# Optimization experiments

Measured on AMD Instinct MI355X. Metric: run time of the kernel, lower is better.

The kernel has to match this reference:

```python
import jax, jax.numpy as jnp
import numpy as np

# ---- config constants (must match init_kwargs) ----
B, S, D, H, HD = 2, 2048, 512, 8, 64
N_BLK, L_BLK = 64, 32          # block_size, block_len (S = N_BLK*L_BLK)
R, RM = 8, 4                   # router_size, group_router_mul_factor
LN, GN, GE, GT = 8, 4, 16, 2   # moe layers, groups, group experts, topk per token
DR, DG = 128, 128
FFH = 1024
THETA = 10000.0
EPS = 1e-6

_INV_FREQ = (1.0 / THETA) ** (np.arange(0, HD, 2, dtype=np.float32) / HD)


def rmsnorm(x, w):
    return x * jax.lax.rsqrt(jnp.mean(x * x, axis=-1, keepdims=True) + EPS) * w


def rope(x):
    # x: (b, h, s, hd); y1 = x1*cos + x2*sin, y2 = -x1*sin + x2*cos (as in RotaryEmb)
    s = x.shape[2]
    freqs = jnp.outer(jnp.arange(s, dtype=jnp.float32), jnp.asarray(_INV_FREQ))[None, None]
    cos, sin = jnp.cos(freqs), jnp.sin(freqs)
    x1, x2 = jnp.split(x, 2, axis=-1)
    return jnp.concatenate([x1 * cos + x2 * sin, -x1 * sin + x2 * cos], axis=-1)


def layer(x, mask, qkv_w, o_w, up_w, down_w, n1, n2):
    b, s, d = x.shape
    xn = rmsnorm(x, n1)
    q, k, v = jnp.split(xn @ qkv_w, 3, axis=-1)
    sh = lambda t: t.reshape(b, s, H, HD).transpose(0, 2, 1, 3)  # b h s hd
    q, k, v = rope(sh(q)), rope(sh(k)), sh(v)
    scores = jnp.einsum('bhqa,bhka->bhqk', q, k) / np.sqrt(HD).astype(np.float32)
    if mask is not None:
        scores = jnp.where(mask[:, None], scores, -jnp.inf)
    p = jax.nn.softmax(scores, axis=-1)
    o = jnp.einsum('bhqk,bhka->bhqa', p, v).transpose(0, 2, 1, 3).reshape(b, s, d)
    x = x + o @ o_w
    xn2 = rmsnorm(x, n2)
    h1, h2 = jnp.split(xn2 @ up_w, 2, axis=-1)
    return x + (jax.nn.silu(h1) * h2) @ down_w


def _l2n(t, axis):
    return t / jnp.maximum(jnp.linalg.norm(t, axis=axis, keepdims=True), 1e-12)


def forward(x, doc, router_token, out_w, keys_router, keys_gate,
            enc_qkv, enc_o, enc_up, enc_down, enc_n1, enc_n2,
            rtr_qkv, rtr_o, rtr_up, rtr_down, rtr_n1, rtr_n2):
    # ---- AuxEncoder: block-causal AND same-document mask (global_attn branch) ----
    qb = jnp.arange(S) // N_BLK
    causal = qb[:, None] >= qb[None, :]                       # (S, S)
    mask = causal[None] & (doc[:, :, None] == doc[:, None, :])  # (B, S, S)
    for i in range(enc_qkv.shape[0]):
        x = layer(x, mask, enc_qkv[i], enc_o[i], enc_up[i], enc_down[i], enc_n1[i], enc_n2[i])

    # ---- AuxRouter: split into blocks, append router tokens, full attention ----
    xr = x.reshape(B * L_BLK, N_BLK, D)
    rt = jnp.broadcast_to(router_token, (B * L_BLK, R, D))
    xr = jnp.concatenate([xr, rt], axis=1)                    # (B*L, N+R, D)
    for i in range(rtr_qkv.shape[0]):
        xr = layer(xr, None, rtr_qkv[i], rtr_o[i], rtr_up[i], rtr_down[i], rtr_n1[i], rtr_n2[i])
    out = xr[:, N_BLK:] @ out_w                               # (B*L, R, DR+DG)
    xro, xgo = out[..., :DR], out[..., DR:]

    def expand(t, dd):
        # repeat '(b l) r d -> (r rm) b l d', roll(1, dim=2), flatten(1,2)
        t = t.reshape(B, L_BLK, R, dd).transpose(2, 0, 1, 3)  # (R, B, L, d)
        t = jnp.repeat(t, RM, axis=0)                          # (R*RM, B, L, d)
        t = jnp.roll(t, 1, axis=2)
        return t.reshape(R * RM, B * L_BLK, dd)

    xrr = _l2n(expand(xro, DR), -1)
    xgg = _l2n(expand(xgo, DG), -1)
    kr = _l2n(keys_router, 1)
    kg = _l2n(keys_gate, 1)
    rl = jnp.einsum('gbd,gde->gbe', xrr, kr)                  # (LN*GN, B*L, GE)
    gl = jnp.einsum('gbd,gde->gbe', xgg, kg)
    _, idx = jax.lax.top_k(rl, GT)                            # (LN*GN, B*L, GT)
    rv = jnp.take_along_axis(rl, idx, axis=-1)
    gv = jnp.take_along_axis(gl, idx, axis=-1)
    return jnp.stack([rv, gv], axis=0)                        # (2, 32, 64, 2)


def setup_inputs() -> dict:
    key = jax.random.key(0)
    ks = jax.random.split(key, 20)
    w = lambda k, shp: 0.02 * jax.random.normal(k, shp, dtype=jnp.float32)
    return {
        'x': jax.random.normal(ks[0], (B, S, D), dtype=jnp.float32),
        'doc': jnp.sort(jax.random.randint(ks[1], (B, S), 0, 4), axis=-1),
        'router_token': jax.random.normal(ks[2], (1, R, D), dtype=jnp.float32),
        'out_w': w(ks[3], (D, DR + DG)),
        'keys_router': jax.random.normal(ks[4], (LN * GN, DR, GE), dtype=jnp.float32),
        'keys_gate': jax.random.normal(ks[5], (LN * GN, DG, GE), dtype=jnp.float32),
        'enc_qkv': w(ks[6], (4, D, 3 * D)),
        'enc_o': w(ks[7], (4, D, D)),
        'enc_up': w(ks[8], (4, D, 2 * FFH)),
        'enc_down': w(ks[9], (4, FFH, D)),
        'enc_n1': jnp.ones((4, D), dtype=jnp.float32),
        'enc_n2': jnp.ones((4, D), dtype=jnp.float32),
        'rtr_qkv': w(ks[10], (2, D, 3 * D)),
        'rtr_o': w(ks[11], (2, D, D)),
        'rtr_up': w(ks[12], (2, D, 2 * FFH)),
        'rtr_down': w(ks[13], (2, FFH, D)),
        'rtr_n1': jnp.ones((2, D), dtype=jnp.float32),
        'rtr_n2': jnp.ones((2, D), dtype=jnp.float32),
    }


def reference(x, doc, router_token, out_w, keys_router, keys_gate,
              enc_qkv, enc_o, enc_up, enc_down, enc_n1, enc_n2,
              rtr_qkv, rtr_o, rtr_up, rtr_down, rtr_n1, rtr_n2):
    return forward(x, doc, router_token, out_w, keys_router, keys_gate,
                   enc_qkv, enc_o, enc_up, enc_down, enc_n1, enc_n2,
                   rtr_qkv, rtr_o, rtr_up, rtr_down, rtr_n1, rtr_n2)
```

## Files before the change

### kernel.cpp

```cpp
#include <hip/hip_runtime.h>
#include <hip/hip_bf16.h>
#include <cstdint>


typedef __attribute__((ext_vector_type(8))) short short8;
typedef __attribute__((ext_vector_type(4))) float f32x4;
typedef unsigned short ushort_t;

__device__ __forceinline__ float bf2f(unsigned short u) {
    return __uint_as_float(((unsigned)u) << 16);
}
__device__ __forceinline__ unsigned short f2bf(float f) {
    unsigned u = __float_as_uint(f);
    unsigned r = 0x7FFFu + ((u >> 16) & 1u);
    return (unsigned short)((u + r) >> 16);
}
__device__ __forceinline__ float wave_sum64(float v) {
#pragma unroll
    for (int o = 32; o; o >>= 1) v += __shfl_xor(v, o);
    return v;
}
__device__ __forceinline__ void load_lds16(const ushort_t* g, ushort_t* l) {
    __builtin_amdgcn_global_load_lds(
        (const __attribute__((address_space(1))) unsigned int*)g,
        (__attribute__((address_space(3))) unsigned int*)l, 16, 0, 0);
}

#define MFMA16(a, b, c) __builtin_amdgcn_mfma_f32_16x16x32_bf16(a, b, c, 0, 0, 0)
#define BARRIER_RAW() do { asm volatile("" ::: "memory"); \
    __builtin_amdgcn_s_barrier(); asm volatile("" ::: "memory"); } while (0)
#define VMCNT0() asm volatile("s_waitcnt vmcnt(0)" ::: "memory")

__global__ void copy_in_kernel(const float* __restrict__ src,
                               float* __restrict__ dst, int n) {
    int i = blockIdx.x * 256 + threadIdx.x;
    if (i < n) dst[i] = src[i];
}

__global__ __launch_bounds__(256) void wsplit_kernel(const float* __restrict__ W,
        unsigned short* __restrict__ WH, unsigned short* __restrict__ WL,
        int K, int N) {
    __shared__ float tile[32][33];
    int bn = blockIdx.x * 32, bk = blockIdx.y * 32;
    int tx = threadIdx.x & 31, ty = threadIdx.x >> 5;
#pragma unroll
    for (int i = 0; i < 4; ++i)
        tile[ty + 8 * i][tx] = W[(size_t)(bk + ty + 8 * i) * N + bn + tx];
    __syncthreads();
#pragma unroll
    for (int i = 0; i < 4; ++i) {
        int n = bn + ty + 8 * i, k = bk + tx;
        float x = tile[tx][ty + 8 * i];
        unsigned short h = f2bf(x);
        unsigned short lo = f2bf(x - bf2f(h));
        WH[(size_t)n * K + k] = h;
        WL[(size_t)n * K + k] = lo;
    }
}

__global__ __launch_bounds__(256) void rmsnorm_kernel(const float* __restrict__ X,
        const float* __restrict__ W, ushort_t* __restrict__ XNH,
        ushort_t* __restrict__ XNL) {
    int t = blockIdx.x, tid = threadIdx.x;
    const float* xr = X + (size_t)t * 512;
    float v0 = xr[tid], v1 = xr[tid + 256];
    float ss = wave_sum64(v0 * v0 + v1 * v1);
    __shared__ float red[4];
    if ((tid & 63) == 0) red[tid >> 6] = ss;
    __syncthreads();
    float tot = red[0] + red[1] + red[2] + red[3];
    float scale = rsqrtf(tot * (1.0f / 512.0f) + 1e-6f);
    float a0 = v0 * scale * W[tid];
    float a1 = v1 * scale * W[tid + 256];
    unsigned short h0 = f2bf(a0), h1 = f2bf(a1);
    size_t base = (size_t)t * 512;
    XNH[base + tid]       = h0;
    XNL[base + tid]       = f2bf(a0 - bf2f(h0));
    XNH[base + tid + 256] = h1;
    XNL[base + tid + 256] = f2bf(a1 - bf2f(h1));
}

template <int BM>
__global__ __launch_bounds__(256) void gemm3(
        const ushort_t* __restrict__ AH, const ushort_t* __restrict__ AL,
        const ushort_t* __restrict__ BH, const ushort_t* __restrict__ BL,
        const float* __restrict__ Res, float* __restrict__ C,
        int M, int N, int K) {
    constexpr int MI   = BM / 32;
    constexpr int ROWS = 2 * BM + 256;
    constexpr int LPW  = ROWS / 64;
    constexpr int SS   = ROWS * 32;
    __shared__ __align__(16) ushort_t S[2][ROWS][32];
    int tid = threadIdx.x;
    int n0 = blockIdx.x * 128, m0 = blockIdx.y * BM;
    int wid = tid >> 6, lane = tid & 63;
    int wm = (wid >> 1) * (BM / 2), wn = (wid & 1) * 64;
    int col = lane & 15, quad = lane >> 4;

    const ushort_t* gsrc[LPW];
    int ldof[LPW];
#pragma unroll
    for (int j = 0; j < LPW; ++j) {
        int e = wid * LPW + j;
        int srow = e * 16 + (lane >> 2);
        const ushort_t* gp; int rin;
        if (srow < BM)                { gp = AH + (size_t)m0 * K; rin = srow; }
        else if (srow < 2 * BM)       { gp = AL + (size_t)m0 * K; rin = srow - BM; }
        else if (srow < 2 * BM + 128) { gp = BH + (size_t)n0 * K; rin = srow - 2 * BM; }
        else                          { gp = BL + (size_t)n0 * K; rin = srow - 2 * BM - 128; }
        gsrc[j] = gp + (size_t)rin * K + ((lane & 3) ^ ((lane >> 3) & 3)) * 8;
        ldof[j] = e * 512;
    }
    ushort_t* sbase = &S[0][0][0];
    auto STAGE = [&](int set, int kc) {
        ushort_t* sb = sbase + set * SS;
#pragma unroll
        for (int j = 0; j < LPW; ++j)
            load_lds16(gsrc[j] + kc * 32, sb + ldof[j]);
    };

    int chrd = (quad ^ ((col >> 1) & 3)) * 8;
    f32x4 acc[MI][4] = {};
    int nk = K >> 5;
    STAGE(0, 0);
    VMCNT0();
    BARRIER_RAW();
    int cur = 0;
#pragma unroll 1
    for (int kc = 0; kc < nk; ++kc) {
        if (kc + 1 < nk) STAGE(cur ^ 1, kc + 1);
        const ushort_t* sb = sbase + cur * SS;
        short8 afh[MI], afl[MI], bfh[4], bfl[4];
#pragma unroll
        for (int i = 0; i < MI; ++i) {
            afh[i] = *(const short8*)(sb + (size_t)(wm + i * 16 + col) * 32 + chrd);
            afl[i] = *(const short8*)(sb + (size_t)(BM + wm + i * 16 + col) * 32 + chrd);
        }
#pragma unroll
        for (int i = 0; i < 4; ++i) {
            bfh[i] = *(const short8*)(sb + (size_t)(2 * BM + wn + i * 16 + col) * 32 + chrd);
            bfl[i] = *(const short8*)(sb + (size_t)(2 * BM + 128 + wn + i * 16 + col) * 32 + chrd);
        }
#pragma unroll
        for (int mi = 0; mi < MI; ++mi)
#pragma unroll
            for (int ni = 0; ni < 4; ++ni) {
                f32x4 c = acc[mi][ni];
                c = MFMA16(afh[mi], bfh[ni], c);
                c = MFMA16(afh[mi], bfl[ni], c);
                c = MFMA16(afl[mi], bfh[ni], c);
                acc[mi][ni] = c;
            }
        if (kc + 1 < nk) {
            VMCNT0();
            BARRIER_RAW();
            cur ^= 1;
        }
    }
#pragma unroll
    for (int mi = 0; mi < MI; ++mi)
#pragma unroll
        for (int ni = 0; ni < 4; ++ni)
#pragma unroll
            for (int r = 0; r < 4; ++r) {
                int row = m0 + wm + mi * 16 + quad * 4 + r;
                int ccol = n0 + wn + ni * 16 + col;
                size_t o = (size_t)row * N + ccol;
                float v = acc[mi][ni][r];
                if (Res) v += Res[o];
                C[o] = v;
            }
}

__global__ __launch_bounds__(256) void gemm_up_silu(
        const ushort_t* __restrict__ AH, const ushort_t* __restrict__ AL,
        const ushort_t* __restrict__ BH, const ushort_t* __restrict__ BL,
        ushort_t* __restrict__ MIDH, ushort_t* __restrict__ MIDL, int K) {
    constexpr int ROWS = 640;
    constexpr int LPW  = 10;
    constexpr int SS   = ROWS * 32;
    __shared__ __align__(16) ushort_t S[2][ROWS][32];
    int tid = threadIdx.x;
    int n0 = blockIdx.x * 128, m0 = blockIdx.y * 64;
    int wid = tid >> 6, lane = tid & 63;
    int wm = (wid >> 1) * 32, wn = (wid & 1) * 64;
    int col = lane & 15, quad = lane >> 4;

    const ushort_t* gsrc[LPW];
    int ldof[LPW];
#pragma unroll
    for (int j = 0; j < LPW; ++j) {
        int e = wid * LPW + j;
        int srow = e * 16 + (lane >> 2);
        const ushort_t* gp; int rin;
        if (srow < 64)       { gp = AH; rin = m0 + srow; }
        else if (srow < 128) { gp = AL; rin = m0 + srow - 64; }
        else if (srow < 256) { gp = BH; rin = n0 + srow - 128; }
        else if (srow < 384) { gp = BL; rin = n0 + srow - 256; }
        else if (srow < 512) { gp = BH; rin = 1024 + n0 + srow - 384; }
        else                 { gp = BL; rin = 1024 + n0 + srow - 512; }
        gsrc[j] = gp + (size_t)rin * K + ((lane & 3) ^ ((lane >> 3) & 3)) * 8;
        ldof[j] = e * 512;
    }
    ushort_t* sbase = &S[0][0][0];
    auto STAGE = [&](int set, int kc) {
        ushort_t* sb = sbase + set * SS;
#pragma unroll
        for (int j = 0; j < LPW; ++j)
            load_lds16(gsrc[j] + kc * 32, sb + ldof[j]);
    };

    int chrd = (quad ^ ((col >> 1) & 3)) * 8;
    f32x4 a1[2][4] = {}, a2[2][4] = {};
    int nk = K >> 5;
    STAGE(0, 0);
    VMCNT0();
    BARRIER_RAW();
    int cur = 0;
#pragma unroll 1
    for (int kc = 0; kc < nk; ++kc) {
        if (kc + 1 < nk) STAGE(cur ^ 1, kc + 1);
        const ushort_t* sb = sbase + cur * SS;
        short8 afh[2], afl[2], b1h[4], b1l[4], b2h[4], b2l[4];
#pragma unroll
        for (int i = 0; i < 2; ++i) {
            afh[i] = *(const short8*)(sb + (size_t)(wm + i * 16 + col) * 32 + chrd);
            afl[i] = *(const short8*)(sb + (size_t)(64 + wm + i * 16 + col) * 32 + chrd);
        }
#pragma unroll
        for (int i = 0; i < 4; ++i) {
            b1h[i] = *(const short8*)(sb + (size_t)(128 + wn + i * 16 + col) * 32 + chrd);
            b1l[i] = *(const short8*)(sb + (size_t)(256 + wn + i * 16 + col) * 32 + chrd);
            b2h[i] = *(const short8*)(sb + (size_t)(384 + wn + i * 16 + col) * 32 + chrd);
            b2l[i] = *(const short8*)(sb + (size_t)(512 + wn + i * 16 + col) * 32 + chrd);
        }
#pragma unroll
        for (int mi = 0; mi < 2; ++mi)
#pragma unroll
            for (int ni = 0; ni < 4; ++ni) {
                f32x4 c = a1[mi][ni];
                c = MFMA16(afh[mi], b1h[ni], c);
                c = MFMA16(afh[mi], b1l[ni], c);
                c = MFMA16(afl[mi], b1h[ni], c);
                a1[mi][ni] = c;
                f32x4 d = a2[mi][ni];
                d = MFMA16(afh[mi], b2h[ni], d);
                d = MFMA16(afh[mi], b2l[ni], d);
                d = MFMA16(afl[mi], b2h[ni], d);
                a2[mi][ni] = d;
            }
        if (kc + 1 < nk) {
            VMCNT0();
            BARRIER_RAW();
            cur ^= 1;
        }
    }
#pragma unroll
    for (int mi = 0; mi < 2; ++mi)
#pragma unroll
        for (int ni = 0; ni < 4; ++ni)
#pragma unroll
            for (int r = 0; r < 4; ++r) {
                int row = m0 + wm + mi * 16 + quad * 4 + r;
                int ccol = n0 + wn + ni * 16 + col;
                float v1 = a1[mi][ni][r], v2 = a2[mi][ni][r];
                float rr = (v1 / (1.0f + __expf(-v1))) * v2;
                unsigned short h = f2bf(rr);
                size_t o = (size_t)row * 1024 + ccol;
                MIDH[o] = h;
                MIDL[o] = f2bf(rr - bf2f(h));
            }
}

__global__ void rope_pack_kernel(const float* __restrict__ QKV,
        float* __restrict__ Q, ushort_t* __restrict__ KH,
        ushort_t* __restrict__ KL, int Sg, int total) {
    int idx = blockIdx.x * 256 + threadIdx.x;
    if (idx >= total) return;
    int i = idx & 31;
    int h = (idx >> 5) & 7;
    int t = idx >> 8;
    int g = t / Sg; int s = t - g * Sg;
    const float* row = QKV + (size_t)t * 1536;
    float inv = powf(10000.0f, -(float)(2 * i) / 64.0f);
    float sn, cs;
    sincosf((float)s * inv, &sn, &cs);
    size_t ob = ((size_t)(g * 8 + h) * Sg + s) * 64 + i;
    int c = h * 64 + i;
    float q1 = row[c], q2 = row[c + 32];
    Q[ob]      = q1 * cs + q2 * sn;
    Q[ob + 32] = q2 * cs - q1 * sn;
    float k1 = row[512 + c], k2 = row[512 + c + 32];
    float ka = k1 * cs + k2 * sn;
    float kb = k2 * cs - k1 * sn;
    unsigned short ha = f2bf(ka), hb = f2bf(kb);
    KH[ob]      = ha;  KL[ob]      = f2bf(ka - bf2f(ha));
    KH[ob + 32] = hb;  KL[ob + 32] = f2bf(kb - bf2f(hb));
}

__global__ __launch_bounds__(256) void vtrans_kernel(const float* __restrict__ QKV,
        ushort_t* __restrict__ VTH, ushort_t* __restrict__ VTL, int Sg) {
    __shared__ float tile[64][65];
    int chunk = blockIdx.x, gh = blockIdx.y;
    int g = gh >> 3, h = gh & 7;
    int tid = threadIdx.x;
    int sr = tid >> 2, dc = (tid & 3) * 16;
    int s = chunk * 64 + sr;
    if (s < Sg) {
        const float* src = QKV + ((size_t)g * Sg + s) * 1536 + 1024 + h * 64 + dc;
#pragma unroll
        for (int j = 0; j < 4; ++j) {
            float4 v = *(const float4*)(src + 4 * j);
            tile[sr][dc + 4 * j]     = v.x;
            tile[sr][dc + 4 * j + 1] = v.y;
            tile[sr][dc + 4 * j + 2] = v.z;
            tile[sr][dc + 4 * j + 3] = v.w;
        }
    } else {
#pragma unroll
        for (int j = 0; j < 16; ++j) tile[sr][dc + j] = 0.f;
    }
    __syncthreads();
    int dr = tid >> 2, sc = (tid & 3) * 16;
    short8 hv[2], lv[2];
#pragma unroll
    for (int half = 0; half < 2; ++half)
#pragma unroll
        for (int j = 0; j < 8; ++j) {
            float v = tile[sc + half * 8 + j][dr];
            unsigned short hb = f2bf(v);
            hv[half][j] = (short)hb;
            lv[half][j] = (short)f2bf(v - bf2f(hb));
        }
    int scol = chunk * 64 + sc;
    size_t ob = ((size_t)gh * 64 + dr) * Sg + scol;
    if (scol + 16 <= Sg) {
        *(short8*)(VTH + ob)     = hv[0];
        *(short8*)(VTH + ob + 8) = hv[1];
        *(short8*)(VTL + ob)     = lv[0];
        *(short8*)(VTL + ob + 8) = lv[1];
    } else {
#pragma unroll
        for (int j = 0; j < 16; ++j)
            if (scol + j < Sg) {
                VTH[ob + j] = (ushort_t)((j < 8) ? hv[0][j] : hv[1][j - 8]);
                VTL[ob + j] = (ushort_t)((j < 8) ? lv[0][j] : lv[1][j - 8]);
            }
    }
}

template <bool MASKED>
__global__ __launch_bounds__(256, 3) void attn3_kernel(const float* __restrict__ Q,
        const ushort_t* __restrict__ KHg, const ushort_t* __restrict__ KLg,
        const ushort_t* __restrict__ VTHg, const ushort_t* __restrict__ VTLg,
        const int* __restrict__ doc, ushort_t* __restrict__ AOH,
        ushort_t* __restrict__ AOL, int Sg) {
    __shared__ __align__(16) ushort_t Khs[64][64], Kls[64][64];
    __shared__ __align__(16) ushort_t Vts[64][64], Vtl[64][64];
    __shared__ __align__(16) ushort_t Ph[4][16][72], Pl[4][16][72];
    __shared__ int dock[64];
    int qb = (int)(gridDim.x - 1 - blockIdx.x);
    int gh = blockIdx.y, g = gh >> 3;
    int tid = threadIdx.x, wid = tid >> 6, lane = tid & 63;
    int col = lane & 15, quad = lane >> 4;

    int rL = lane >> 3, cSw = (lane & 7) ^ rL;
    const ushort_t* kb;
    const ushort_t* vb;
    ushort_t* lb;
    if (wid == 0)      { kb = KHg + (size_t)gh * Sg * 64 + cSw * 8;  vb = nullptr; lb = &Khs[0][0]; }
    else if (wid == 1) { kb = KLg + (size_t)gh * Sg * 64 + cSw * 8;  vb = nullptr; lb = &Kls[0][0]; }
    else if (wid == 2) { vb = VTHg + ((size_t)gh * 64 + rL) * Sg;    kb = nullptr; lb = &Vts[0][0]; }
    else               { vb = VTLg + ((size_t)gh * 64 + rL) * Sg;    kb = nullptr; lb = &Vtl[0][0]; }
    int sw0 = ((0 + quad) ^ (col & 7)) * 8;
    int sw1 = ((4 + quad) ^ (col & 7)) * 8;

    short8 qa[2][2];
    {
        int qrow = qb * 64 + wid * 16 + col;
        if (qrow >= Sg) qrow = Sg - 1;
        const float* Qg = Q + ((size_t)gh * Sg + qrow) * 64 + quad * 8;
#pragma unroll
        for (int kk = 0; kk < 2; ++kk) {
            float4 v0 = *(const float4*)(Qg + kk * 32);
            float4 v1 = *(const float4*)(Qg + kk * 32 + 4);
            float vv[8] = {v0.x, v0.y, v0.z, v0.w, v1.x, v1.y, v1.z, v1.w};
            short8 h, l;
#pragma unroll
            for (int e = 0; e < 8; ++e) {
                float x = vv[e] * 0.125f;
                unsigned short hb = f2bf(x);
                h[e] = (short)hb;
                l[e] = (short)f2bf(x - bf2f(hb));
            }
            qa[kk][0] = h; qa[kk][1] = l;
        }
    }
    int dqr[4]; int wq0 = 0, wq1 = 0, bq0 = 0, bq1 = 0;
    if (MASKED) {
        const int* db = doc + (size_t)g * Sg + qb * 64;
#pragma unroll
        for (int r = 0; r < 4; ++r) dqr[r] = db[wid * 16 + quad * 4 + r];
        wq0 = db[wid * 16]; wq1 = db[wid * 16 + 15];
        bq0 = db[0];        bq1 = db[63];
    }
    float m[4], l[4];
    f32x4 accO[4];
#pragma unroll
    for (int r = 0; r < 4; ++r) { m[r] = -1e30f; l[r] = 0.f; }
#pragma unroll
    for (int nd = 0; nd < 4; ++nd) accO[nd] = (f32x4){0.f, 0.f, 0.f, 0.f};

    int nkt = MASKED ? (qb + 1) : ((Sg + 63) >> 6);
    for (int kt = 0; kt < nkt; ++kt) {
        int kval = Sg - kt * 64; if (kval > 64) kval = 64;
        __syncthreads();
        if (MASKED) {
            if (tid < 64) dock[tid] = doc[(size_t)g * Sg + kt * 64 + tid];
            __syncthreads();
        }
        bool bskip = false;
        if (MASKED) bskip = (dock[63] < bq0) || (dock[0] > bq1);
        if (!bskip) {
            if (wid < 2) {
#pragma unroll
                for (int p = 0; p < 8; ++p) {
                    int sr2 = kt * 64 + p * 8 + rL;
                    if (sr2 > Sg - 1) sr2 = Sg - 1;
                    load_lds16(kb + (size_t)sr2 * 64, lb + p * 512);
                }
            } else {
                int vc = kt * 64 + cSw * 8;
                if (vc > Sg - 8) vc = Sg - 8;
#pragma unroll
                for (int p = 0; p < 8; ++p)
                    load_lds16(vb + (size_t)(p * 8) * Sg + vc, lb + p * 512);
            }
            __syncthreads();
            bool wskip = false;
            if (MASKED) wskip = (dock[kval - 1] < wq0) || (dock[0] > wq1);
            if (!wskip) {
                int dk[4];
                if (MASKED) {
#pragma unroll
                    for (int ni = 0; ni < 4; ++ni) dk[ni] = dock[ni * 16 + col];
                }
                f32x4 sc[4];
#pragma unroll
                for (int ni = 0; ni < 4; ++ni) {
                    int rb = (ni * 16 + col) * 64;
                    short8 bh0 = *(const short8*)(&Khs[0][0] + rb + sw0);
                    short8 bl0 = *(const short8*)(&Kls[0][0] + rb + sw0);
                    short8 bh1 = *(const short8*)(&Khs[0][0] + rb + sw1);
                    short8 bl1 = *(const short8*)(&Kls[0][0] + rb + sw1);
                    f32x4 c = (f32x4){0.f, 0.f, 0.f, 0.f};
                    c = MFMA16(qa[0][0], bh0, c);
                    c = MFMA16(qa[0][0], bl0, c);
                    c = MFMA16(qa[0][1], bh0, c);
                    c = MFMA16(qa[1][0], bh1, c);
                    c = MFMA16(qa[1][0], bl1, c);
                    c = MFMA16(qa[1][1], bh1, c);
                    sc[ni] = c;
                }
                float mnew[4];
#pragma unroll
                for (int r = 0; r < 4; ++r) mnew[r] = -1e30f;
#pragma unroll
                for (int ni = 0; ni < 4; ++ni)
#pragma unroll
                    for (int r = 0; r < 4; ++r) {
                        bool ok = MASKED ? (dk[ni] == dqr[r]) : (ni * 16 + col < kval);
                        float s = ok ? sc[ni][r] : -1e30f;
                        sc[ni][r] = s;
                        mnew[r] = fmaxf(mnew[r], s);
                    }
#pragma unroll
                for (int r = 0; r < 4; ++r)
#pragma unroll
                    for (int o = 1; o < 16; o <<= 1)
                        mnew[r] = fmaxf(mnew[r], __shfl_xor(mnew[r], o));
                float alpha[4], lsum[4];
#pragma unroll
                for (int r = 0; r < 4; ++r) {
                    float M = fmaxf(m[r], mnew[r]);
                    alpha[r] = __expf(m[r] - M);
                    m[r] = M;
                    lsum[r] = 0.f;
                }
#pragma unroll
                for (int ni = 0; ni < 4; ++ni)
#pragma unroll
                    for (int r = 0; r < 4; ++r) {
                        bool ok = MASKED ? (dk[ni] == dqr[r]) : (ni * 16 + col < kval);
                        float p = ok ? __expf(sc[ni][r] - m[r]) : 0.f;
                        lsum[r] += p;
                        unsigned short h = f2bf(p);
                        Ph[wid][quad * 4 + r][ni * 16 + col] = h;
                        Pl[wid][quad * 4 + r][ni * 16 + col] = f2bf(p - bf2f(h));
                    }
#pragma unroll
                for (int r = 0; r < 4; ++r) {
#pragma unroll
                    for (int o = 1; o < 16; o <<= 1)
                        lsum[r] += __shfl_xor(lsum[r], o);
                    l[r] = l[r] * alpha[r] + lsum[r];
                }
#pragma unroll
                for (int nd = 0; nd < 4; ++nd)
#pragma unroll
                    for (int r = 0; r < 4; ++r) accO[nd][r] *= alpha[r];
#pragma unroll
                for (int kk = 0; kk < 2; ++kk) {
                    short8 pah = *(const short8*)&Ph[wid][col][kk * 32 + quad * 8];
                    short8 pal = *(const short8*)&Pl[wid][col][kk * 32 + quad * 8];
                    int sw = kk ? sw1 : sw0;
#pragma unroll
                    for (int nd = 0; nd < 4; ++nd) {
                        int rb = (nd * 16 + col) * 64;
                        short8 vbh = *(const short8*)(&Vts[0][0] + rb + sw);
                        short8 vbl = *(const short8*)(&Vtl[0][0] + rb + sw);
                        f32x4 c = accO[nd];
                        c = MFMA16(pah, vbh, c);
                        c = MFMA16(pah, vbl, c);
                        c = MFMA16(pal, vbh, c);
                        accO[nd] = c;
                    }
                }
            }
        }
    }
#pragma unroll
    for (int r = 0; r < 4; ++r) {
        int qrow = qb * 64 + wid * 16 + quad * 4 + r;
        if (qrow < Sg) {
            float inv = 1.0f / l[r];
            size_t base = ((size_t)g * Sg + qrow) * 512 + (gh & 7) * 64;
#pragma unroll
            for (int nd = 0; nd < 4; ++nd) {
                float val = accO[nd][r] * inv;
                unsigned short h = f2bf(val);
                AOH[base + nd * 16 + col] = h;
                AOL[base + nd * 16 + col] = f2bf(val - bf2f(h));
            }
        }
    }
}

__global__ void router_build_kernel(const float* __restrict__ X,
        const float* __restrict__ RT, float* __restrict__ X2, int total) {
    int idx = blockIdx.x * 256 + threadIdx.x;
    if (idx >= total) return;
    int d = idx & 511;
    int p = (idx >> 9) % 72;
    int g2 = idx / (72 * 512);
    X2[idx] = (p < 64) ? X[((size_t)g2 * 64 + p) * 512 + d]
                       : RT[(p - 64) * 512 + d];
}

__global__ void gather_rows_kernel(const float* __restrict__ X2,
        ushort_t* __restrict__ RRH, ushort_t* __restrict__ RRL, int total) {
    int idx = blockIdx.x * 256 + threadIdx.x;
    if (idx >= total) return;
    int d = idx & 511;
    int row = idx >> 9;
    int g2 = row >> 3, rr = row & 7;
    float v = X2[((size_t)(g2 * 72 + 64 + rr)) * 512 + d];
    unsigned short h = f2bf(v);
    RRH[idx] = h;
    RRL[idx] = f2bf(v - bf2f(h));
}

__global__ __launch_bounds__(64) void norm_half_kernel(const float* __restrict__ IN,
        float* __restrict__ OUT) {
    int b = blockIdx.x; int lane = threadIdx.x;
    size_t base = (size_t)(b >> 1) * 256 + (size_t)(b & 1) * 128;
    float v0 = IN[base + lane], v1 = IN[base + 64 + lane];
    float ss = wave_sum64(v0 * v0 + v1 * v1);
    float sc = 1.0f / fmaxf(sqrtf(ss), 1e-12f);
    OUT[base + lane]      = v0 * sc;
    OUT[base + 64 + lane] = v1 * sc;
}

__global__ __launch_bounds__(64) void norm_keys_kernel(const float* __restrict__ Kin,
        float* __restrict__ Kout) {
    int b = blockIdx.x; int lane = threadIdx.x;
    int g = b >> 4, e = b & 15;
    size_t base = (size_t)g * 2048 + e;
    float v0 = Kin[base + (size_t)lane * 16];
    float v1 = Kin[base + (size_t)(lane + 64) * 16];
    float ss = wave_sum64(v0 * v0 + v1 * v1);
    float sc = 1.0f / fmaxf(sqrtf(ss), 1e-12f);
    Kout[base + (size_t)lane * 16]        = v0 * sc;
    Kout[base + (size_t)(lane + 64) * 16] = v1 * sc;
}

__global__ __launch_bounds__(64) void logits_top2_kernel(const float* __restrict__ OUTN,
        const float* __restrict__ KRN, const float* __restrict__ KGN,
        float* __restrict__ out) {
    int blk = blockIdx.x;
    int g = blk >> 6, bcol = blk & 63;
    int b = bcol >> 5, l = bcol & 31;
    int lsrc = (l + 31) & 31;
    int r = g >> 2;
    int row = (b * 32 + lsrc) * 8 + r;
    const float* rvec = OUTN + (size_t)row * 256;
    __shared__ float sc[32];
    int lane = threadIdx.x;
    if (lane < 32) {
        int e = lane & 15;
        const float* kb = ((lane < 16) ? KRN : KGN) + (size_t)g * 2048 + e;
        const float* xv = (lane < 16) ? rvec : (rvec + 128);
        float s = 0.f;
#pragma unroll 8
        for (int d = 0; d < 128; ++d) s = fmaf(xv[d], kb[(size_t)d * 16], s);
        sc[lane] = s;
    }
    __syncthreads();
    if (lane == 0) {
        float bv = -1e30f, sv = -1e30f; int bi = 0, si = 0;
#pragma unroll
        for (int e = 0; e < 16; ++e) {
            float v = sc[e];
            if (v > bv) { sv = bv; si = bi; bv = v; bi = e; }
            else if (v > sv) { sv = v; si = e; }
        }
        size_t base = (size_t)g * 128 + (size_t)bcol * 2;
        out[base]            = bv;
        out[base + 1]        = sv;
        out[4096 + base]     = sc[16 + bi];
        out[4096 + base + 1] = sc[16 + si];
    }
}

static void run_layer(float* X, float* BIG, float* Qb,
                      ushort_t* KHb, ushort_t* KLb, ushort_t* VTHb, ushort_t* VTLb,
                      ushort_t* XNH, ushort_t* XNL, ushort_t* AOH, ushort_t* AOL,
                      ushort_t* MIDH, ushort_t* MIDL,
                      const unsigned short* WH, const unsigned short* WL,
                      const float* n1, const float* n2,
                      const int* doc, int G, int Sg, hipStream_t stream) {
    const size_t oQKV = 0, oO = 786432, oUP = 1048576, oDN = 2097152;
    int T = G * Sg;
    rmsnorm_kernel<<<T, 256, 0, stream>>>(X, n1, XNH, XNL);
    gemm3<64><<<dim3(12, T / 64), 256, 0, stream>>>(XNH, XNL, WH + oQKV, WL + oQKV, nullptr, BIG, T, 1536, 512);
    int rp = T * 256;
    rope_pack_kernel<<<(rp + 255) / 256, 256, 0, stream>>>(BIG, Qb, KHb, KLb, Sg, rp);
    int qblocks = (Sg + 63) >> 6;
    vtrans_kernel<<<dim3(qblocks, G * 8), 256, 0, stream>>>(BIG, VTHb, VTLb, Sg);
    if (doc)
        attn3_kernel<true><<<dim3(qblocks, G * 8), 256, 0, stream>>>(Qb, KHb, KLb, VTHb, VTLb, doc, AOH, AOL, Sg);
    else
        attn3_kernel<false><<<dim3(qblocks, G * 8), 256, 0, stream>>>(Qb, KHb, KLb, VTHb, VTLb, nullptr, AOH, AOL, Sg);
    gemm3<64><<<dim3(4, T / 64), 256, 0, stream>>>(AOH, AOL, WH + oO, WL + oO, X, X, T, 512, 512);
    rmsnorm_kernel<<<T, 256, 0, stream>>>(X, n2, XNH, XNL);
    gemm_up_silu<<<dim3(8, T / 64), 256, 0, stream>>>(XNH, XNL, WH + oUP, WL + oUP, MIDH, MIDL, 512);
    gemm3<64><<<dim3(4, T / 64), 256, 0, stream>>>(MIDH, MIDL, WH + oDN, WL + oDN, X, X, T, 512, 1024);
}

static void split_layer(const float* qkv, const float* o, const float* up, const float* dn,
                        unsigned short* WH, unsigned short* WL, hipStream_t stream) {
    const size_t oQKV = 0, oO = 786432, oUP = 1048576, oDN = 2097152;
    wsplit_kernel<<<dim3(48, 16), 256, 0, stream>>>(qkv, WH + oQKV, WL + oQKV, 512, 1536);
    wsplit_kernel<<<dim3(16, 16), 256, 0, stream>>>(o,   WH + oO,   WL + oO,   512, 512);
    wsplit_kernel<<<dim3(64, 16), 256, 0, stream>>>(up,  WH + oUP,  WL + oUP,  512, 2048);
    wsplit_kernel<<<dim3(16, 32), 256, 0, stream>>>(dn,  WH + oDN,  WL + oDN,  1024, 512);
}

extern "C" void kernel_launch(void* const* d_in, const int* in_sizes, int n_in,
                              void* d_out, int out_size, void* d_ws, size_t ws_size,
                              hipStream_t stream) {
    const float* x_in    = (const float*)d_in[0];
    const int*   doc     = (const int*)d_in[1];
    const float* rt      = (const float*)d_in[2];
    const float* out_w   = (const float*)d_in[3];
    const float* k_rt    = (const float*)d_in[4];
    const float* k_gt    = (const float*)d_in[5];
    const float* enc_qkv = (const float*)d_in[6];
    const float* enc_o   = (const float*)d_in[7];
    const float* enc_up  = (const float*)d_in[8];
    const float* enc_dn  = (const float*)d_in[9];
    const float* enc_n1  = (const float*)d_in[10];
    const float* enc_n2  = (const float*)d_in[11];
    const float* rtr_qkv = (const float*)d_in[12];
    const float* rtr_o   = (const float*)d_in[13];
    const float* rtr_up  = (const float*)d_in[14];
    const float* rtr_dn  = (const float*)d_in[15];
    const float* rtr_n1  = (const float*)d_in[16];
    const float* rtr_n2  = (const float*)d_in[17];

    float* ws = (float*)d_ws;
    size_t off = 0;
    auto alloc = [&](size_t n) { float* p = ws + off; off += n; return p; };
    float* X    = alloc(4608UL * 512);
    float* X2   = alloc(4608UL * 512);
    float* BIG  = alloc(4608UL * 2048);
    float* Qb   = alloc(4608UL * 512);
    ushort_t* KHb  = (ushort_t*)alloc(1179648UL);
    ushort_t* KLb  = (ushort_t*)alloc(1179648UL);
    ushort_t* VTHb = (ushort_t*)alloc(1179648UL);
    ushort_t* VTLb = (ushort_t*)alloc(1179648UL);
    unsigned short* WH = (unsigned short*)(ws + off);
    unsigned short* WL = WH + 2621440UL;
    off += 2621440UL;
    ushort_t* XNH = (ushort_t*)Qb;
    ushort_t* XNL = XNH + 4608UL * 512;
    ushort_t* AOH = (ushort_t*)BIG;
    ushort_t* AOL = AOH + 4608UL * 512;
    ushort_t* MIDH = (ushort_t*)BIG;
    ushort_t* MIDL = MIDH + 4608UL * 1024;
    ushort_t* RRH = (ushort_t*)X;
    ushort_t* RRL = RRH + 262144;
    float* OUTM = X + 262144;
    float* OUTN = X + 393216;
    float* KRN  = X + 524288;
    float* KGN  = X + 589824;
    (void)ws_size; (void)in_sizes; (void)n_in; (void)out_size;

    copy_in_kernel<<<(2097152 + 255) / 256, 256, 0, stream>>>(x_in, X, 2097152);

    for (int i = 0; i < 4; ++i) {
        split_layer(enc_qkv + (size_t)i * 512 * 1536,
                    enc_o   + (size_t)i * 512 * 512,
                    enc_up  + (size_t)i * 512 * 2048,
                    enc_dn  + (size_t)i * 1024 * 512, WH, WL, stream);
        run_layer(X, BIG, Qb, KHb, KLb, VTHb, VTLb, XNH, XNL, AOH, AOL, MIDH, MIDL,
                  WH, WL, enc_n1 + (size_t)i * 512, enc_n2 + (size_t)i * 512,
                  doc, 2, 2048, stream);
    }

    int rb_total = 64 * 72 * 512;
    router_build_kernel<<<(rb_total + 255) / 256, 256, 0, stream>>>(X, rt, X2, rb_total);

    for (int i = 0; i < 2; ++i) {
        split_layer(rtr_qkv + (size_t)i * 512 * 1536,
                    rtr_o   + (size_t)i * 512 * 512,
                    rtr_up  + (size_t)i * 512 * 2048,
                    rtr_dn  + (size_t)i * 1024 * 512, WH, WL, stream);
        run_layer(X2, BIG, Qb, KHb, KLb, VTHb, VTLb, XNH, XNL, AOH, AOL, MIDH, MIDL,
                  WH, WL, rtr_n1 + (size_t)i * 512, rtr_n2 + (size_t)i * 512,
                  nullptr, 64, 72, stream);
    }

    gather_rows_kernel<<<(512 * 512) / 256, 256, 0, stream>>>(X2, RRH, RRL, 512 * 512);
    wsplit_kernel<<<dim3(8, 16), 256, 0, stream>>>(out_w, WH, WL, 512, 256);
    gemm3<64><<<dim3(2, 8), 256, 0, stream>>>(RRH, RRL, WH, WL, nullptr, OUTM, 512, 256, 512);

    norm_half_kernel<<<1024, 64, 0, stream>>>(OUTM, OUTN);
    norm_keys_kernel<<<512, 64, 0, stream>>>(k_rt, KRN);
    norm_keys_kernel<<<512, 64, 0, stream>>>(k_gt, KGN);
    logits_top2_kernel<<<2048, 64, 0, stream>>>(OUTN, KRN, KGN, (float*)d_out);
}
```

Baseline: 1.300 ms.

## Load GEMM A-operand fragments directly into registers, shrink LDS tiles

The GEMM kernels now fetch the activation (A) hi/lo fragments straight from global memory into registers, prefetching one k-step ahead, and stage only the weight (B) tiles through LDS. The N tile shrinks for the output, down and up projections, so more blocks launch and each block uses much less LDS, which should raise occupancy and parallelism. The cost is uncoalesced 16-byte per-lane global reads for A, and each A row is now fetched by several blocks and by both waves of a block that share it, with no LDS reuse.

After: 1.577 ms. 21.3% more time.

```diff
diff --git a/kernel.cpp b/kernel.cpp
--- a/kernel.cpp
+++ b/kernel.cpp
@@ -80,21 +80,21 @@
     XNL[base + tid + 256] = f2bf(a1 - bf2f(h1));
 }
 
-template <int BM>
-__global__ __launch_bounds__(256) void gemm3(
+template <int BN>
+__global__ __launch_bounds__(256) void gemm3r(
         const ushort_t* __restrict__ AH, const ushort_t* __restrict__ AL,
         const ushort_t* __restrict__ BH, const ushort_t* __restrict__ BL,
         const float* __restrict__ Res, float* __restrict__ C,
         int M, int N, int K) {
-    constexpr int MI   = BM / 32;
-    constexpr int ROWS = 2 * BM + 256;
+    constexpr int NI   = BN / 32;
+    constexpr int ROWS = 2 * BN;
     constexpr int LPW  = ROWS / 64;
     constexpr int SS   = ROWS * 32;
     __shared__ __align__(16) ushort_t S[2][ROWS][32];
     int tid = threadIdx.x;
-    int n0 = blockIdx.x * 128, m0 = blockIdx.y * BM;
+    int n0 = blockIdx.x * BN, m0 = blockIdx.y * 64;
     int wid = tid >> 6, lane = tid & 63;
-    int wm = (wid >> 1) * (BM / 2), wn = (wid & 1) * 64;
+    int wm = (wid >> 1) * 32, wn = (wid & 1) * (BN / 2);
     int col = lane & 15, quad = lane >> 4;
 
     const ushort_t* gsrc[LPW];
@@ -104,12 +104,18 @@
         int e = wid * LPW + j;
         int srow = e * 16 + (lane >> 2);
         const ushort_t* gp; int rin;
-        if (srow < BM)                { gp = AH + (size_t)m0 * K; rin = srow; }
-        else if (srow < 2 * BM)       { gp = AL + (size_t)m0 * K; rin = srow - BM; }
-        else if (srow < 2 * BM + 128) { gp = BH + (size_t)n0 * K; rin = srow - 2 * BM; }
-        else                          { gp = BL + (size_t)n0 * K; rin = srow - 2 * BM - 128; }
+        if (srow < BN) { gp = BH; rin = n0 + srow; }
+        else           { gp = BL; rin = n0 + srow - BN; }
         gsrc[j] = gp + (size_t)rin * K + ((lane & 3) ^ ((lane >> 3) & 3)) * 8;
         ldof[j] = e * 512;
+    }
+    const ushort_t* apH[2];
+    const ushort_t* apL[2];
+#pragma unroll
+    for (int mi = 0; mi < 2; ++mi) {
+        int arow = m0 + wm + mi * 16 + col;
+        apH[mi] = AH + (size_t)arow * K + quad * 8;
+        apL[mi] = AL + (size_t)arow * K + quad * 8;
     }
     ushort_t* sbase = &S[0][0][0];
     auto STAGE = [&](int set, int kc) {
@@ -120,47 +126,57 @@
     };
 
     int chrd = (quad ^ ((col >> 1) & 3)) * 8;
-    f32x4 acc[MI][4] = {};
+    f32x4 acc[2][NI] = {};
     int nk = K >> 5;
+    short8 aCH[2], aCL[2], aNH[2], aNL[2];
+#pragma unroll
+    for (int mi = 0; mi < 2; ++mi) {
+        aCH[mi] = *(const short8*)(apH[mi]);
+        aCL[mi] = *(const short8*)(apL[mi]);
+    }
     STAGE(0, 0);
     VMCNT0();
     BARRIER_RAW();
     int cur = 0;
 #pragma unroll 1
     for (int kc = 0; kc < nk; ++kc) {
-        if (kc + 1 < nk) STAGE(cur ^ 1, kc + 1);
+        if (kc + 1 < nk) {
+            STAGE(cur ^ 1, kc + 1);
+#pragma unroll
+            for (int mi = 0; mi < 2; ++mi) {
+                aNH[mi] = *(const short8*)(apH[mi] + (kc + 1) * 32);
+                aNL[mi] = *(const short8*)(apL[mi] + (kc + 1) * 32);
+            }
+        }
         const ushort_t* sb = sbase + cur * SS;
-        short8 afh[MI], afl[MI], bfh[4], bfl[4];
-#pragma unroll
-        for (int i = 0; i < MI; ++i) {
-            afh[i] = *(const short8*)(sb + (size_t)(wm + i * 16 + col) * 32 + chrd);
-            afl[i] = *(const short8*)(sb + (size_t)(BM + wm + i * 16 + col) * 32 + chrd);
-        }
-#pragma unroll
-        for (int i = 0; i < 4; ++i) {
-            bfh[i] = *(const short8*)(sb + (size_t)(2 * BM + wn + i * 16 + col) * 32 + chrd);
-            bfl[i] = *(const short8*)(sb + (size_t)(2 * BM + 128 + wn + i * 16 + col) * 32 + chrd);
-        }
-#pragma unroll
-        for (int mi = 0; mi < MI; ++mi)
-#pragma unroll
-            for (int ni = 0; ni < 4; ++ni) {
+        short8 bfh[NI], bfl[NI];
+#pragma unroll
+        for (int i = 0; i < NI; ++i) {
+            bfh[i] = *(const short8*)(sb + (size_t)(wn + i * 16 + col) * 32 + chrd);
+            bfl[i] = *(const short8*)(sb + (size_t)(BN + wn + i * 16 + col) * 32 + chrd);
+        }
+#pragma unroll
+        for (int mi = 0; mi < 2; ++mi)
+#pragma unroll
+            for (int ni = 0; ni < NI; ++ni) {
                 f32x4 c = acc[mi][ni];
-                c = MFMA16(afh[mi], bfh[ni], c);
-                c = MFMA16(afh[mi], bfl[ni], c);
-                c = MFMA16(afl[mi], bfh[ni], c);
+                c = MFMA16(aCH[mi], bfh[ni], c);
+                c = MFMA16(aCH[mi], bfl[ni], c);
+                c = MFMA16(aCL[mi], bfh[ni], c);
                 acc[mi][ni] = c;
             }
         if (kc + 1 < nk) {
             VMCNT0();
             BARRIER_RAW();
             cur ^= 1;
-        }
-    }
-#pragma unroll
-    for (int mi = 0; mi < MI; ++mi)
-#pragma unroll
-        for (int ni = 0; ni < 4; ++ni)
+#pragma unroll
+            for (int mi = 0; mi < 2; ++mi) { aCH[mi] = aNH[mi]; aCL[mi] = aNL[mi]; }
+        }
+    }
+#pragma unroll
+    for (int mi = 0; mi < 2; ++mi)
+#pragma unroll
+        for (int ni = 0; ni < NI; ++ni)
 #pragma unroll
             for (int r = 0; r < 4; ++r) {
                 int row = m0 + wm + mi * 16 + quad * 4 + r;
@@ -176,14 +192,14 @@
         const ushort_t* __restrict__ AH, const ushort_t* __restrict__ AL,
         const ushort_t* __restrict__ BH, const ushort_t* __restrict__ BL,
         ushort_t* __restrict__ MIDH, ushort_t* __restrict__ MIDL, int K) {
-    constexpr int ROWS = 640;
-    constexpr int LPW  = 10;
+    constexpr int ROWS = 256;
+    constexpr int LPW  = 4;
     constexpr int SS   = ROWS * 32;
     __shared__ __align__(16) ushort_t S[2][ROWS][32];
     int tid = threadIdx.x;
-    int n0 = blockIdx.x * 128, m0 = blockIdx.y * 64;
+    int n0 = blockIdx.x * 64, m0 = blockIdx.y * 64;
     int wid = tid >> 6, lane = tid & 63;
-    int wm = (wid >> 1) * 32, wn = (wid & 1) * 64;
+    int wm = (wid >> 1) * 32, wn = (wid & 1) * 32;
     int col = lane & 15, quad = lane >> 4;
 
     const ushort_t* gsrc[LPW];
@@ -193,14 +209,20 @@
         int e = wid * LPW + j;
         int srow = e * 16 + (lane >> 2);
         const ushort_t* gp; int rin;
-        if (srow < 64)       { gp = AH; rin = m0 + srow; }
-        else if (srow < 128) { gp = AL; rin = m0 + srow - 64; }
-        else if (srow < 256) { gp = BH; rin = n0 + srow - 128; }
-        else if (srow < 384) { gp = BL; rin = n0 + srow - 256; }
-        else if (srow < 512) { gp = BH; rin = 1024 + n0 + srow - 384; }
-        else                 { gp = BL; rin = 1024 + n0 + srow - 512; }
+        if (srow < 64)       { gp = BH; rin = n0 + srow; }
+        else if (srow < 128) { gp = BL; rin = n0 + srow - 64; }
+        else if (srow < 192) { gp = BH; rin = 1024 + n0 + srow - 128; }
+        else                 { gp = BL; rin = 1024 + n0 + srow - 192; }
         gsrc[j] = gp + (size_t)rin * K + ((lane & 3) ^ ((lane >> 3) & 3)) * 8;
         ldof[j] = e * 512;
+    }
+    const ushort_t* apH[2];
+    const ushort_t* apL[2];
+#pragma unroll
+    for (int mi = 0; mi < 2; ++mi) {
+        int arow = m0 + wm + mi * 16 + col;
+        apH[mi] = AH + (size_t)arow * K + quad * 8;
+        apL[mi] = AL + (size_t)arow * K + quad * 8;
     }
     ushort_t* sbase = &S[0][0][0];
     auto STAGE = [&](int set, int kc) {
@@ -211,54 +233,64 @@
     };
 
     int chrd = (quad ^ ((col >> 1) & 3)) * 8;
-    f32x4 a1[2][4] = {}, a2[2][4] = {};
+    f32x4 a1[2][2] = {}, a2[2][2] = {};
     int nk = K >> 5;
+    short8 aCH[2], aCL[2], aNH[2], aNL[2];
+#pragma unroll
+    for (int mi = 0; mi < 2; ++mi) {
+        aCH[mi] = *(const short8*)(apH[mi]);
+        aCL[mi] = *(const short8*)(apL[mi]);
+    }
     STAGE(0, 0);
     VMCNT0();
     BARRIER_RAW();
     int cur = 0;
 #pragma unroll 1
     for (int kc = 0; kc < nk; ++kc) {
-        if (kc + 1 < nk) STAGE(cur ^ 1, kc + 1);
+        if (kc + 1 < nk) {
+            STAGE(cur ^ 1, kc + 1);
+#pragma unroll
+            for (int mi = 0; mi < 2; ++mi) {
+                aNH[mi] = *(const short8*)(apH[mi] + (kc + 1) * 32);
+                aNL[mi] = *(const short8*)(apL[mi] + (kc + 1) * 32);
+            }
+        }
         const ushort_t* sb = sbase + cur * SS;
-        short8 afh[2], afl[2], b1h[4], b1l[4], b2h[4], b2l[4];
+        short8 b1h[2], b1l[2], b2h[2], b2l[2];
 #pragma unroll
         for (int i = 0; i < 2; ++i) {
-            afh[i] = *(const short8*)(sb + (size_t)(wm + i * 16 + col) * 32 + chrd);
-            afl[i] = *(const short8*)(sb + (size_t)(64 + wm + i * 16 + col) * 32 + chrd);
-        }
-#pragma unroll
-        for (int i = 0; i < 4; ++i) {
-            b1h[i] = *(const short8*)(sb + (size_t)(128 + wn + i * 16 + col) * 32 + chrd);
-            b1l[i] = *(const short8*)(sb + (size_t)(256 + wn + i * 16 + col) * 32 + chrd);
-            b2h[i] = *(const short8*)(sb + (size_t)(384 + wn + i * 16 + col) * 32 + chrd);
-            b2l[i] = *(const short8*)(sb + (size_t)(512 + wn + i * 16 + col) * 32 + chrd);
+            b1h[i] = *(const short8*)(sb + (size_t)(wn + i * 16 + col) * 32 + chrd);
+            b1l[i] = *(const short8*)(sb + (size_t)(64 + wn + i * 16 + col) * 32 + chrd);
+            b2h[i] = *(const short8*)(sb + (size_t)(128 + wn + i * 16 + col) * 32 + chrd);
+            b2l[i] = *(const short8*)(sb + (size_t)(192 + wn + i * 16 + col) * 32 + chrd);
         }
 #pragma unroll
         for (int mi = 0; mi < 2; ++mi)
 #pragma unroll
-            for (int ni = 0; ni < 4; ++ni) {
+            for (int ni = 0; ni < 2; ++ni) {
                 f32x4 c = a1[mi][ni];
-                c = MFMA16(afh[mi], b1h[ni], c);
-                c = MFMA16(afh[mi], b1l[ni], c);
-                c = MFMA16(afl[mi], b1h[ni], c);
+                c = MFMA16(aCH[mi], b1h[ni], c);
+                c = MFMA16(aCH[mi], b1l[ni], c);
+                c = MFMA16(aCL[mi], b1h[ni], c);
                 a1[mi][ni] = c;
                 f32x4 d = a2[mi][ni];
-                d = MFMA16(afh[mi], b2h[ni], d);
-                d = MFMA16(afh[mi], b2l[ni], d);
-                d = MFMA16(afl[mi], b2h[ni], d);
+                d = MFMA16(aCH[mi], b2h[ni], d);
+                d = MFMA16(aCH[mi], b2l[ni], d);
+                d = MFMA16(aCL[mi], b2h[ni], d);
                 a2[mi][ni] = d;
             }
         if (kc + 1 < nk) {
             VMCNT0();
             BARRIER_RAW();
             cur ^= 1;
+#pragma unroll
+            for (int mi = 0; mi < 2; ++mi) { aCH[mi] = aNH[mi]; aCL[mi] = aNL[mi]; }
         }
     }
 #pragma unroll
     for (int mi = 0; mi < 2; ++mi)
 #pragma unroll
-        for (int ni = 0; ni < 4; ++ni)
+        for (int ni = 0; ni < 2; ++ni)
 #pragma unroll
             for (int r = 0; r < 4; ++r) {
                 int row = m0 + wm + mi * 16 + quad * 4 + r;
@@ -642,7 +674,7 @@
     const size_t oQKV = 0, oO = 786432, oUP = 1048576, oDN = 2097152;
     int T = G * Sg;
     rmsnorm_kernel<<<T, 256, 0, stream>>>(X, n1, XNH, XNL);
-    gemm3<64><<<dim3(12, T / 64), 256, 0, stream>>>(XNH, XNL, WH + oQKV, WL + oQKV, nullptr, BIG, T, 1536, 512);
+    gemm3r<128><<<dim3(12, T / 64), 256, 0, stream>>>(XNH, XNL, WH + oQKV, WL + oQKV, nullptr, BIG, T, 1536, 512);
     int rp = T * 256;
     rope_pack_kernel<<<(rp + 255) / 256, 256, 0, stream>>>(BIG, Qb, KHb, KLb, Sg, rp);
     int qblocks = (Sg + 63) >> 6;
@@ -651,10 +683,10 @@
         attn3_kernel<true><<<dim3(qblocks, G * 8), 256, 0, stream>>>(Qb, KHb, KLb, VTHb, VTLb, doc, AOH, AOL, Sg);
     else
         attn3_kernel<false><<<dim3(qblocks, G * 8), 256, 0, stream>>>(Qb, KHb, KLb, VTHb, VTLb, nullptr, AOH, AOL, Sg);
-    gemm3<64><<<dim3(4, T / 64), 256, 0, stream>>>(AOH, AOL, WH + oO, WL + oO, X, X, T, 512, 512);
+    gemm3r<64><<<dim3(8, T / 64), 256, 0, stream>>>(AOH, AOL, WH + oO, WL + oO, X, X, T, 512, 512);
     rmsnorm_kernel<<<T, 256, 0, stream>>>(X, n2, XNH, XNL);
-    gemm_up_silu<<<dim3(8, T / 64), 256, 0, stream>>>(XNH, XNL, WH + oUP, WL + oUP, MIDH, MIDL, 512);
-    gemm3<64><<<dim3(4, T / 64), 256, 0, stream>>>(MIDH, MIDL, WH + oDN, WL + oDN, X, X, T, 512, 1024);
+    gemm_up_silu<<<dim3(16, T / 64), 256, 0, stream>>>(XNH, XNL, WH + oUP, WL + oUP, MIDH, MIDL, 512);
+    gemm3r<64><<<dim3(8, T / 64), 256, 0, stream>>>(MIDH, MIDL, WH + oDN, WL + oDN, X, X, T, 512, 1024);
 }
 
 static void split_layer(const float* qkv, const float* o, const float* up, const float* dn,
@@ -743,7 +775,7 @@
 
     gather_rows_kernel<<<(512 * 512) / 256, 256, 0, stream>>>(X2, RRH, RRL, 512 * 512);
     wsplit_kernel<<<dim3(8, 16), 256, 0, stream>>>(out_w, WH, WL, 512, 256);
-    gemm3<64><<<dim3(2, 8), 256, 0, stream>>>(RRH, RRL, WH, WL, nullptr, OUTM, 512, 256, 512);
+    gemm3r<64><<<dim3(4, 8), 256, 0, stream>>>(RRH, RRL, WH, WL, nullptr, OUTM, 512, 256, 512);
 
     norm_half_kernel<<<1024, 64, 0, stream>>>(OUTM, OUTN);
     norm_keys_kernel<<<512, 64, 0, stream>>>(k_rt, KRN);
```
